# Kernel tuning notes

Measured on AMD Instinct MI355X. Metric: run time of the kernel, lower is better.

Reference implementation:

```python
import jax, jax.numpy as jnp
import numpy as np

BN_EPS = 1e-5

def _maxpool2x2(t):
    # t: [B, C, H, W] -> [B, C, H//2, W//2]
    B, C, H, W = t.shape
    return t.reshape(B, C, H // 2, 2, W // 2, 2).max(axis=(3, 5))

def setup_inputs() -> dict:
    key = jax.random.key(0)
    ks = jax.random.split(key, 7)
    B, C, D, H, W = 16, 256, 128, 64, 64
    return {
        "x": jax.random.normal(ks[0], (B, C, H, W), dtype=jnp.float32),
        "g_w": jax.random.normal(ks[1], (D, C), dtype=jnp.float32) * (1.0 / np.sqrt(C)),
        "g_b": jax.random.normal(ks[2], (D,), dtype=jnp.float32) * 0.01,
        "w_w": jax.random.normal(ks[3], (C, D), dtype=jnp.float32) * (1.0 / np.sqrt(D)),
        "w_b": jax.random.normal(ks[4], (C,), dtype=jnp.float32) * 0.01,
        "gamma": jax.random.normal(ks[5], (C,), dtype=jnp.float32),
        "beta": jax.random.normal(ks[6], (C,), dtype=jnp.float32),
    }

def reference(x, g_w, g_b, w_w, w_b, gamma, beta):
    B, C, H, W = x.shape
    D = g_w.shape[0]
    # g branch: 1x1 conv C->D then 2x2 maxpool, flatten -> [B, M, D]
    g_x = jnp.einsum('bchw,dc->bdhw', x, g_w) + g_b[None, :, None, None]
    g_x = _maxpool2x2(g_x).reshape(B, D, -1).transpose(0, 2, 1)      # [B, M, D]
    # theta: raw x flattened -> [B, N, C]; phi: maxpooled x -> [B, C, M]
    theta = x.reshape(B, C, -1).transpose(0, 2, 1)                    # [B, N, C]
    phi = _maxpool2x2(x).reshape(B, C, -1)                            # [B, C, M]
    f = jnp.einsum('bnc,bcm->bnm', theta, phi)                        # [B, N, M]
    attn = jax.nn.softmax(f, axis=-1)
    y = jnp.einsum('bnm,bmd->bnd', attn, g_x)                         # [B, N, D]
    y = y.transpose(0, 2, 1).reshape(B, D, H, W)
    # W: 1x1 conv D->C then BatchNorm2d (training mode: batch stats)
    w_y = jnp.einsum('bdhw,cd->bchw', y, w_w) + w_b[None, :, None, None]
    mean = w_y.mean(axis=(0, 2, 3))
    var = w_y.var(axis=(0, 2, 3))  # biased, matching torch BN normalization
    w_y = (w_y - mean[None, :, None, None]) * jax.lax.rsqrt(var + BN_EPS)[None, :, None, None]
    w_y = w_y * gamma[None, :, None, None] + beta[None, :, None, None]
    return w_y + x
```

## Files before the change

### kernel.cpp

```cpp
#include <hip/hip_runtime.h>
#include <hip/hip_bf16.h>

typedef _Float16 half8 __attribute__((ext_vector_type(8)));
typedef float f32x4 __attribute__((ext_vector_type(4)));
typedef unsigned uint4e __attribute__((ext_vector_type(4)));

#define B_ 16
#define C_ 256
#define D_ 128
#define H_ 64
#define W_ 64
#define N_ 4096
#define M_ 1024
#define NCH 32

static constexpr size_t WS_PHI   = 0;
static constexpr size_t WS_GPOOL = WS_PHI   + (size_t)B_*M_*C_*2;
static constexpr size_t WS_Y     = WS_GPOOL + (size_t)B_*D_*M_*2;
static constexpr size_t WS_BNSUM = WS_Y     + (size_t)B_*N_*D_*2;
static constexpr size_t WS_BNSSQ = WS_BNSUM + (size_t)C_*4;
static constexpr size_t WS_PSUM  = WS_BNSSQ + (size_t)C_*4;
static constexpr size_t WS_PSSQ  = WS_PSUM  + (size_t)256*256*4;
static constexpr size_t WS_GW16  = WS_PSSQ  + (size_t)256*256*4;
static constexpr size_t WS_WW16  = WS_GW16  + (size_t)D_*C_*2;

typedef __attribute__((address_space(3))) void lds_vt;
typedef const __attribute__((address_space(1))) void gbl_vt;

__device__ __forceinline__ void gl2lds16(const void* g, void* s) {
  __builtin_amdgcn_global_load_lds((gbl_vt*)g, (lds_vt*)s, 16, 0, 0);
}

__device__ __forceinline__ unsigned pkrtz(float a, float b) {
  auto v = __builtin_amdgcn_cvt_pkrtz(a, b);
  return __builtin_bit_cast(unsigned, v);
}

__global__ __launch_bounds__(256) void conv16_kernel(
    const float* __restrict__ gw, const float* __restrict__ ww,
    _Float16* __restrict__ gw16, _Float16* __restrict__ ww16) {
  const int i = blockIdx.x*256 + threadIdx.x;
  gw16[i] = (_Float16)gw[i];
  ww16[i] = (_Float16)ww[i];
}

__global__ __launch_bounds__(256) void fused_pre_kernel(
    const float* __restrict__ x, const _Float16* __restrict__ gw16,
    const float* __restrict__ g_b, _Float16* __restrict__ phi,
    _Float16* __restrict__ gpool) {
  const int i = blockIdx.x;
  const int b = blockIdx.y;
  const int t = threadIdx.x;
  const int w = t >> 6, l = t & 63, gq = l >> 4, c16 = l & 15;
  const float* xb = x + (size_t)b*C_*N_;

  f32x4 acc[8][2];
#pragma unroll
  for (int ds = 0; ds < 8; ++ds) {
    acc[ds][0] = (f32x4){0.f,0.f,0.f,0.f};
    acc[ds][1] = (f32x4){0.f,0.f,0.f,0.f};
  }

  const int n0 = i*128 + w*16 + c16;
  const int mrow = i*32 + w*8 + (c16 >> 1);

  for (int kk = 0; kk < 8; ++kk) {
    const int c0 = kk*32 + gq*8;
    half8 bf0, bf1;
#pragma unroll
    for (int j = 0; j < 8; ++j) {
      bf0[j] = (_Float16)xb[(size_t)(c0 + j)*N_ + n0];
      bf1[j] = (_Float16)xb[(size_t)(c0 + j)*N_ + n0 + 64];
    }
    half8 pk_;
#pragma unroll
    for (int j = 0; j < 8; ++j) {
      float v = fmaxf((float)bf0[j], (float)bf1[j]);
      v = fmaxf(v, __shfl_xor(v, 1, 64));
      pk_[j] = (_Float16)v;
    }
    if (!(l & 1))
      *(half8*)(phi + ((size_t)b*M_ + mrow)*C_ + c0) = pk_;
#pragma unroll
    for (int ds = 0; ds < 8; ++ds) {
      half8 af = *(const half8*)(gw16 + (size_t)(ds*16 + c16)*C_ + c0);
      acc[ds][0] = __builtin_amdgcn_mfma_f32_16x16x32_f16(af, bf0, acc[ds][0], 0, 0, 0);
      acc[ds][1] = __builtin_amdgcn_mfma_f32_16x16x32_f16(af, bf1, acc[ds][1], 0, 0, 0);
    }
  }

#pragma unroll
  for (int ds = 0; ds < 8; ++ds) {
#pragma unroll
    for (int r = 0; r < 4; ++r) {
      const int d = ds*16 + gq*4 + r;
      float v = fmaxf(acc[ds][0][r], acc[ds][1][r]);
      v = fmaxf(v, __shfl_xor(v, 1, 64));
      if (!(l & 1))
        gpool[((size_t)b*D_ + d)*M_ + mrow] = (_Float16)(v + g_b[d]);
    }
  }
}

__device__ __forceinline__ half8 build_pa(const float p0[4], const float p1[4], int gq) {
  unsigned d0 = pkrtz(p0[0], p0[1]);
  unsigned d1 = pkrtz(p0[2], p0[3]);
  unsigned e0 = pkrtz(p1[0], p1[1]);
  unsigned e1 = pkrtz(p1[2], p1[3]);
  unsigned D0 = __shfl_xor(d0, 16, 64), D1 = __shfl_xor(d1, 16, 64);
  unsigned E0 = __shfl_xor(e0, 16, 64), E1 = __shfl_xor(e1, 16, 64);
  const bool lo = gq < 2;
  unsigned s0 = lo ? e0 : d0, s1 = lo ? e1 : d1;
  unsigned s2 = lo ? E0 : D0, s3 = lo ? E1 : D1;
  unsigned R0 = __shfl_xor(s0, 32, 64), R1 = __shfl_xor(s1, 32, 64);
  unsigned R2 = __shfl_xor(s2, 32, 64), R3 = __shfl_xor(s3, 32, 64);
  uint4e u;
  u[0] = gq==0 ? d0 : gq==1 ? R2 : gq==2 ? R0 : E0;
  u[1] = gq==0 ? d1 : gq==1 ? R3 : gq==2 ? R1 : E1;
  u[2] = gq==0 ? D0 : gq==1 ? R0 : gq==2 ? R2 : e0;
  u[3] = gq==0 ? D1 : gq==1 ? R1 : gq==2 ? R3 : e1;
  return __builtin_bit_cast(half8, u);
}

__global__ __launch_bounds__(256, 2) void attn_kernel(
    const float* __restrict__ x, const _Float16* __restrict__ phi,
    const _Float16* __restrict__ gpool, _Float16* __restrict__ y) {
  const int nt = blockIdx.x;
  const int b  = blockIdx.y;
  const int t  = threadIdx.x;
  const int w = t >> 6, l = t & 63, gq = l >> 4, c16 = l & 15;
  const int nw = nt*128 + w*32;

  __shared__ alignas(16) _Float16 phi_s[2][32*256];
  __shared__ alignas(16) _Float16 gp_s[2][128*32];

  half8 qf[2][8];
#pragma unroll
  for (int rt = 0; rt < 2; ++rt) {
    const int nq = nw + rt*16 + c16;
#pragma unroll
    for (int kk = 0; kk < 8; ++kk) {
      const int cb = kk*32 + gq*8;
      half8 q;
#pragma unroll
      for (int j = 0; j < 8; ++j) q[j] = (_Float16)x[((size_t)b*C_ + cb + j)*N_ + nq];
      qf[rt][kk] = q;
    }
  }

  f32x4 yacc[2][8];
#pragma unroll
  for (int rt = 0; rt < 2; ++rt)
#pragma unroll
    for (int ds = 0; ds < 8; ++ds) yacc[rt][ds] = (f32x4){0.f,0.f,0.f,0.f};
  float m_run[2] = {-INFINITY, -INFINITY};
  float l_run[2] = {0.f, 0.f};

  const int lhi = l >> 5, l31 = l & 31;

  auto stage = [&](int buf, int ch2) {
    const int m0 = ch2 * 32;
#pragma unroll
    for (int jj = 0; jj < 4; ++jj) {
      const int j = w*4 + jj;
      const char* src = (const char*)phi + ((size_t)(b*M_ + m0 + l31))*512 + (2*j + lhi)*16;
      gl2lds16(src, (char*)&phi_s[buf][0] + j*1024);
    }
#pragma unroll
    for (int jj = 0; jj < 2; ++jj) {
      const int j = w*2 + jj;
      const char* src = (const char*)gpool + (((size_t)(b*D_ + (j&1)*64 + l))*M_ + m0)*2 + (j>>1)*16;
      gl2lds16(src, (char*)&gp_s[buf][0] + j*1024);
    }
  };

  stage(0, 0);

  const char* pAbase = (const char*)&phi_s[0][0] + gq*512 + c16*16;
  const char* pBbase = (const char*)&gp_s[0][0] + gq*2048 + c16*16;

  for (int ch = 0; ch < NCH; ++ch) {
    const int cur = ch & 1;
    if (ch + 1 < NCH) {
      stage(cur ^ 1, ch + 1);
      asm volatile("s_waitcnt vmcnt(6)" ::: "memory");
    } else {
      asm volatile("s_waitcnt vmcnt(0)" ::: "memory");
    }
    __builtin_amdgcn_s_barrier();
    asm volatile("" ::: "memory");

    f32x4 fS[2][2];
    fS[0][0] = (f32x4){0.f,0.f,0.f,0.f}; fS[0][1] = (f32x4){0.f,0.f,0.f,0.f};
    fS[1][0] = (f32x4){0.f,0.f,0.f,0.f}; fS[1][1] = (f32x4){0.f,0.f,0.f,0.f};
    const char* pA = pAbase + cur*16384;
    __builtin_amdgcn_s_setprio(1);
#pragma unroll
    for (int kk = 0; kk < 8; ++kk) {
      half8 a0 = *(const half8*)(pA + kk*2048);
      half8 a1 = *(const half8*)(pA + kk*2048 + 256);
      fS[0][0] = __builtin_amdgcn_mfma_f32_16x16x32_f16(a0, qf[0][kk], fS[0][0], 0, 0, 0);
      fS[1][0] = __builtin_amdgcn_mfma_f32_16x16x32_f16(a0, qf[1][kk], fS[1][0], 0, 0, 0);
      fS[0][1] = __builtin_amdgcn_mfma_f32_16x16x32_f16(a1, qf[0][kk], fS[0][1], 0, 0, 0);
      fS[1][1] = __builtin_amdgcn_mfma_f32_16x16x32_f16(a1, qf[1][kk], fS[1][1], 0, 0, 0);
    }
    __builtin_amdgcn_s_setprio(0);

    float cm[2];
#pragma unroll
    for (int rt = 0; rt < 2; ++rt) {
      float cmax = fS[rt][0][0];
#pragma unroll
      for (int mt = 0; mt < 2; ++mt)
#pragma unroll
        for (int r = 0; r < 4; ++r) cmax = fmaxf(cmax, fS[rt][mt][r]);
      cmax = fmaxf(cmax, __shfl_xor(cmax, 16, 64));
      cmax = fmaxf(cmax, __shfl_xor(cmax, 32, 64));
      cm[rt] = cmax;
    }
    const float grow = fmaxf(cm[0] - m_run[0], cm[1] - m_run[1]);
    if (__any(grow > 8.0f)) {
#pragma unroll
      for (int rt = 0; rt < 2; ++rt) {
        const float mn = fmaxf(m_run[rt], cm[rt]);
        const float sc = __expf(m_run[rt] - mn);
        m_run[rt] = mn;
        l_run[rt] *= sc;
        const int sci = __float_as_int(sc);
#pragma unroll
        for (int r = 0; r < 4; ++r) {
          const float scn = __int_as_float(__builtin_amdgcn_ds_bpermute(4*(gq*4 + r), sci));
#pragma unroll
          for (int ds = 0; ds < 8; ++ds) yacc[rt][ds][r] *= scn;
        }
      }
    }
    half8 pa[2];
#pragma unroll
    for (int rt = 0; rt < 2; ++rt) {
      float p0[4], p1[4];
      float rs = 0.f;
#pragma unroll
      for (int r = 0; r < 4; ++r) {
        p0[r] = __expf(fS[rt][0][r] - m_run[rt]);
        p1[r] = __expf(fS[rt][1][r] - m_run[rt]);
        rs += p0[r] + p1[r];
      }
      rs += __shfl_xor(rs, 16, 64);
      rs += __shfl_xor(rs, 32, 64);
      l_run[rt] += rs;
      pa[rt] = build_pa(p0, p1, gq);
    }

    const char* pB = pBbase + cur*8192;
    __builtin_amdgcn_s_setprio(1);
#pragma unroll
    for (int ds = 0; ds < 8; ++ds) {
      half8 bv = *(const half8*)(pB + ds*256);
      yacc[0][ds] = __builtin_amdgcn_mfma_f32_16x16x32_f16(pa[0], bv, yacc[0][ds], 0, 0, 0);
      yacc[1][ds] = __builtin_amdgcn_mfma_f32_16x16x32_f16(pa[1], bv, yacc[1][ds], 0, 0, 0);
    }
    __builtin_amdgcn_s_setprio(0);

    asm volatile("" ::: "memory");
    __builtin_amdgcn_s_barrier();
    asm volatile("" ::: "memory");
  }

#pragma unroll
  for (int rt = 0; rt < 2; ++rt) {
    const float inv = 1.0f / l_run[rt];
    const int invi = __float_as_int(inv);
#pragma unroll
    for (int r = 0; r < 4; ++r) {
      const float invn = __int_as_float(__builtin_amdgcn_ds_bpermute(4*(gq*4 + r), invi));
      const int n = nw + rt*16 + gq*4 + r;
      _Float16* yr = y + ((size_t)b*N_ + n)*D_ + c16;
#pragma unroll
      for (int ds = 0; ds < 8; ++ds) yr[ds*16] = (_Float16)(yacc[rt][ds][r] * invn);
    }
  }
}

__global__ __launch_bounds__(256) void stats_partial_kernel(
    const _Float16* __restrict__ y, const _Float16* __restrict__ ww16,
    const float* __restrict__ w_b, float* __restrict__ psum,
    float* __restrict__ pssq) {
  const int nt = blockIdx.x, b = blockIdx.y, t = threadIdx.x;
  const int w = t >> 6, l = t & 63, g = l >> 4, c16 = l & 15;

  float s_acc[4][4], q_acc[4][4], wb_r[4][4];
#pragma unroll
  for (int cs = 0; cs < 4; ++cs)
#pragma unroll
    for (int r = 0; r < 4; ++r) {
      s_acc[cs][r] = 0.f; q_acc[cs][r] = 0.f;
      wb_r[cs][r] = w_b[w*64 + cs*16 + g*4 + r];
    }

  for (int nb = 0; nb < 4; ++nb) {
    const int n0 = nt*256 + nb*64;
    f32x4 acc[4][4];
#pragma unroll
    for (int a = 0; a < 4; ++a)
#pragma unroll
      for (int n = 0; n < 4; ++n) acc[a][n] = (f32x4){0.f,0.f,0.f,0.f};

#pragma unroll
    for (int kk = 0; kk < 4; ++kk) {
      const int d0 = kk*32 + g*8;
      half8 af[4];
#pragma unroll
      for (int cs = 0; cs < 4; ++cs)
        af[cs] = *(const half8*)(ww16 + (size_t)(w*64 + cs*16 + c16)*D_ + d0);
#pragma unroll
      for (int ns = 0; ns < 4; ++ns) {
        const int nn = n0 + ns*16 + c16;
        half8 bf = *(const half8*)&y[((size_t)b*N_ + nn)*D_ + d0];
#pragma unroll
        for (int cs = 0; cs < 4; ++cs)
          acc[cs][ns] = __builtin_amdgcn_mfma_f32_16x16x32_f16(af[cs], bf, acc[cs][ns], 0, 0, 0);
      }
    }
#pragma unroll
    for (int cs = 0; cs < 4; ++cs)
#pragma unroll
      for (int r = 0; r < 4; ++r) {
        const float wb = wb_r[cs][r];
#pragma unroll
        for (int ns = 0; ns < 4; ++ns) {
          const float v = acc[cs][ns][r] + wb;
          s_acc[cs][r] += v; q_acc[cs][r] += v*v;
        }
      }
  }

  const int blk = b*16 + nt;
#pragma unroll
  for (int cs = 0; cs < 4; ++cs)
#pragma unroll
    for (int r = 0; r < 4; ++r) {
      float s = s_acc[cs][r], q = q_acc[cs][r];
      s += __shfl_xor(s, 1, 64); s += __shfl_xor(s, 2, 64);
      s += __shfl_xor(s, 4, 64); s += __shfl_xor(s, 8, 64);
      q += __shfl_xor(q, 1, 64); q += __shfl_xor(q, 2, 64);
      q += __shfl_xor(q, 4, 64); q += __shfl_xor(q, 8, 64);
      if (c16 == 0) {
        const int c = w*64 + cs*16 + g*4 + r;
        psum[blk*C_ + c] = s;
        pssq[blk*C_ + c] = q;
      }
    }
}

__global__ __launch_bounds__(256) void stats_reduce_kernel(
    const float* __restrict__ psum, const float* __restrict__ pssq,
    float* __restrict__ bnsum, float* __restrict__ bnssq) {
  const int t = threadIdx.x;
  const int ci = t & 31, bi = t >> 5;
  const int c = blockIdx.x*32 + ci;
  float s = 0.f, q = 0.f;
  for (int k = 0; k < 32; ++k) {
    const int row = bi + k*8;
    s += psum[row*C_ + c];
    q += pssq[row*C_ + c];
  }
  __shared__ float rs[8][32], rq[8][32];
  rs[bi][ci] = s; rq[bi][ci] = q;
  __syncthreads();
  if (bi == 0) {
    float S = 0.f, Q = 0.f;
#pragma unroll
    for (int k2 = 0; k2 < 8; ++k2) { S += rs[k2][ci]; Q += rq[k2][ci]; }
    bnsum[c] = S; bnssq[c] = Q;
  }
}

__global__ __launch_bounds__(256) void wconv_bn_kernel(
    const _Float16* __restrict__ y, const _Float16* __restrict__ ww16,
    const float* __restrict__ w_b, const float* __restrict__ bnsum,
    const float* __restrict__ bnssq, const float* __restrict__ gamma,
    const float* __restrict__ beta, const float* __restrict__ x,
    float* __restrict__ out) {
  const int nt = blockIdx.x, b = blockIdx.y, t = threadIdx.x;
  const int w = t >> 6, l = t & 63, g = l >> 4, c16 = l & 15;
  const int n0 = nt*64;

  f32x4 acc[4][4];
#pragma unroll
  for (int a = 0; a < 4; ++a)
#pragma unroll
    for (int n = 0; n < 4; ++n) acc[a][n] = (f32x4){0.f,0.f,0.f,0.f};

#pragma unroll
  for (int kk = 0; kk < 4; ++kk) {
    const int d0 = kk*32 + g*8;
    half8 af[4];
#pragma unroll
    for (int cs = 0; cs < 4; ++cs)
      af[cs] = *(const half8*)(ww16 + (size_t)(w*64 + cs*16 + c16)*D_ + d0);
#pragma unroll
    for (int ns = 0; ns < 4; ++ns) {
      const int nn = n0 + ns*16 + c16;
      half8 bf = *(const half8*)&y[((size_t)b*N_ + nn)*D_ + d0];
#pragma unroll
      for (int cs = 0; cs < 4; ++cs)
        acc[cs][ns] = __builtin_amdgcn_mfma_f32_16x16x32_f16(af[cs], bf, acc[cs][ns], 0, 0, 0);
    }
  }

  const float inv_cnt = 1.0f / (float)((size_t)B_ * N_);
#pragma unroll
  for (int cs = 0; cs < 4; ++cs) {
#pragma unroll
    for (int r = 0; r < 4; ++r) {
      const int c = w*64 + cs*16 + g*4 + r;
      const float wb  = w_b[c];
      const float mean = bnsum[c] * inv_cnt;
      const float var  = bnssq[c] * inv_cnt - mean*mean;
      const float istd = rsqrtf(var + 1e-5f);
      const float ga = gamma[c], be = beta[c];
#pragma unroll
      for (int ns = 0; ns < 4; ++ns) {
        const int n = n0 + ns*16 + c16;
        const size_t idx = ((size_t)b*C_ + c)*N_ + n;
        const float v = acc[cs][ns][r] + wb;
        out[idx] = (v - mean)*istd*ga + be + x[idx];
      }
    }
  }
}

extern "C" void kernel_launch(void* const* d_in, const int* in_sizes, int n_in,
                              void* d_out, int out_size, void* d_ws, size_t ws_size,
                              hipStream_t stream) {
  const float* x     = (const float*)d_in[0];
  const float* g_w   = (const float*)d_in[1];
  const float* g_b   = (const float*)d_in[2];
  const float* w_w   = (const float*)d_in[3];
  const float* w_b   = (const float*)d_in[4];
  const float* gamma = (const float*)d_in[5];
  const float* beta  = (const float*)d_in[6];
  float* out = (float*)d_out;

  char* ws = (char*)d_ws;
  _Float16* phi   = (_Float16*)(ws + WS_PHI);
  _Float16* gpool = (_Float16*)(ws + WS_GPOOL);
  _Float16* yb    = (_Float16*)(ws + WS_Y);
  float*    bnsum = (float*)(ws + WS_BNSUM);
  float*    bnssq = (float*)(ws + WS_BNSSQ);
  float*    psum  = (float*)(ws + WS_PSUM);
  float*    pssq  = (float*)(ws + WS_PSSQ);
  _Float16* gw16  = (_Float16*)(ws + WS_GW16);
  _Float16* ww16  = (_Float16*)(ws + WS_WW16);

  conv16_kernel<<<128, 256, 0, stream>>>(g_w, w_w, gw16, ww16);
  fused_pre_kernel<<<dim3(32, 16), 256, 0, stream>>>(x, gw16, g_b, phi, gpool);
  attn_kernel<<<dim3(32, 16), 256, 0, stream>>>(x, phi, gpool, yb);
  stats_partial_kernel<<<dim3(16, 16), 256, 0, stream>>>(yb, ww16, w_b, psum, pssq);
  stats_reduce_kernel<<<8, 256, 0, stream>>>(psum, pssq, bnsum, bnssq);
  wconv_bn_kernel<<<dim3(64, 16), 256, 0, stream>>>(yb, ww16, w_b, bnsum, bnssq, gamma, beta, x, out);
}
```

Before: 228.8 us.

## Double warps per block and shrink per-warp tiles across pre, attention and stats kernels

Result: slower. 283.2 us (+23.8%).

```diff
diff --git a/kernel.cpp b/kernel.cpp
--- a/kernel.cpp
+++ b/kernel.cpp
@@ -20,8 +20,8 @@
 static constexpr size_t WS_BNSUM = WS_Y     + (size_t)B_*N_*D_*2;
 static constexpr size_t WS_BNSSQ = WS_BNSUM + (size_t)C_*4;
 static constexpr size_t WS_PSUM  = WS_BNSSQ + (size_t)C_*4;
-static constexpr size_t WS_PSSQ  = WS_PSUM  + (size_t)256*256*4;
-static constexpr size_t WS_GW16  = WS_PSSQ  + (size_t)256*256*4;
+static constexpr size_t WS_PSSQ  = WS_PSUM  + (size_t)1024*256*4;
+static constexpr size_t WS_GW16  = WS_PSSQ  + (size_t)1024*256*4;
 static constexpr size_t WS_WW16  = WS_GW16  + (size_t)D_*C_*2;
 
 typedef __attribute__((address_space(3))) void lds_vt;
@@ -44,25 +44,26 @@
   ww16[i] = (_Float16)ww[i];
 }
 
-__global__ __launch_bounds__(256) void fused_pre_kernel(
+__global__ __launch_bounds__(512, 4) void fused_pre_kernel(
     const float* __restrict__ x, const _Float16* __restrict__ gw16,
     const float* __restrict__ g_b, _Float16* __restrict__ phi,
     _Float16* __restrict__ gpool) {
   const int i = blockIdx.x;
   const int b = blockIdx.y;
   const int t = threadIdx.x;
-  const int w = t >> 6, l = t & 63, gq = l >> 4, c16 = l & 15;
+  const int w = t >> 6, l = t & 63, gq = (l >> 4) & 3, c16 = l & 15;
+  const int wn = w & 3, wd = w >> 2;
   const float* xb = x + (size_t)b*C_*N_;
 
-  f32x4 acc[8][2];
-#pragma unroll
-  for (int ds = 0; ds < 8; ++ds) {
+  f32x4 acc[4][2];
+#pragma unroll
+  for (int ds = 0; ds < 4; ++ds) {
     acc[ds][0] = (f32x4){0.f,0.f,0.f,0.f};
     acc[ds][1] = (f32x4){0.f,0.f,0.f,0.f};
   }
 
-  const int n0 = i*128 + w*16 + c16;
-  const int mrow = i*32 + w*8 + (c16 >> 1);
+  const int n0 = i*128 + wn*16 + c16;
+  const int mrow = i*32 + wn*8 + (c16 >> 1);
 
   for (int kk = 0; kk < 8; ++kk) {
     const int c0 = kk*32 + gq*8;
@@ -72,28 +73,30 @@
       bf0[j] = (_Float16)xb[(size_t)(c0 + j)*N_ + n0];
       bf1[j] = (_Float16)xb[(size_t)(c0 + j)*N_ + n0 + 64];
     }
-    half8 pk_;
-#pragma unroll
-    for (int j = 0; j < 8; ++j) {
-      float v = fmaxf((float)bf0[j], (float)bf1[j]);
-      v = fmaxf(v, __shfl_xor(v, 1, 64));
-      pk_[j] = (_Float16)v;
-    }
-    if (!(l & 1))
-      *(half8*)(phi + ((size_t)b*M_ + mrow)*C_ + c0) = pk_;
-#pragma unroll
-    for (int ds = 0; ds < 8; ++ds) {
-      half8 af = *(const half8*)(gw16 + (size_t)(ds*16 + c16)*C_ + c0);
+    if (wd == 0) {
+      half8 pk_;
+#pragma unroll
+      for (int j = 0; j < 8; ++j) {
+        float v = fmaxf((float)bf0[j], (float)bf1[j]);
+        v = fmaxf(v, __shfl_xor(v, 1, 64));
+        pk_[j] = (_Float16)v;
+      }
+      if (!(l & 1))
+        *(half8*)(phi + ((size_t)b*M_ + mrow)*C_ + c0) = pk_;
+    }
+#pragma unroll
+    for (int ds = 0; ds < 4; ++ds) {
+      half8 af = *(const half8*)(gw16 + (size_t)((wd*4 + ds)*16 + c16)*C_ + c0);
       acc[ds][0] = __builtin_amdgcn_mfma_f32_16x16x32_f16(af, bf0, acc[ds][0], 0, 0, 0);
       acc[ds][1] = __builtin_amdgcn_mfma_f32_16x16x32_f16(af, bf1, acc[ds][1], 0, 0, 0);
     }
   }
 
 #pragma unroll
-  for (int ds = 0; ds < 8; ++ds) {
+  for (int ds = 0; ds < 4; ++ds) {
 #pragma unroll
     for (int r = 0; r < 4; ++r) {
-      const int d = ds*16 + gq*4 + r;
+      const int d = (wd*4 + ds)*16 + gq*4 + r;
       float v = fmaxf(acc[ds][0][r], acc[ds][1][r]);
       v = fmaxf(v, __shfl_xor(v, 1, 64));
       if (!(l & 1))
@@ -122,144 +125,120 @@
   return __builtin_bit_cast(half8, u);
 }
 
-__global__ __launch_bounds__(256, 2) void attn_kernel(
+__global__ __launch_bounds__(512, 4) void attn_kernel(
     const float* __restrict__ x, const _Float16* __restrict__ phi,
     const _Float16* __restrict__ gpool, _Float16* __restrict__ y) {
   const int nt = blockIdx.x;
   const int b  = blockIdx.y;
   const int t  = threadIdx.x;
-  const int w = t >> 6, l = t & 63, gq = l >> 4, c16 = l & 15;
-  const int nw = nt*128 + w*32;
+  const int w = t >> 6, l = t & 63, gq = (l >> 4) & 3, c16 = l & 15;
 
   __shared__ alignas(16) _Float16 phi_s[2][32*256];
-  __shared__ alignas(16) _Float16 gp_s[2][128*32];
-
-  half8 qf[2][8];
-#pragma unroll
-  for (int rt = 0; rt < 2; ++rt) {
-    const int nq = nw + rt*16 + c16;
+
+  half8 qf[8];
+  {
+    const int nq = nt*128 + w*16 + c16;
 #pragma unroll
     for (int kk = 0; kk < 8; ++kk) {
       const int cb = kk*32 + gq*8;
       half8 q;
 #pragma unroll
       for (int j = 0; j < 8; ++j) q[j] = (_Float16)x[((size_t)b*C_ + cb + j)*N_ + nq];
-      qf[rt][kk] = q;
-    }
-  }
-
-  f32x4 yacc[2][8];
-#pragma unroll
-  for (int rt = 0; rt < 2; ++rt)
-#pragma unroll
-    for (int ds = 0; ds < 8; ++ds) yacc[rt][ds] = (f32x4){0.f,0.f,0.f,0.f};
-  float m_run[2] = {-INFINITY, -INFINITY};
-  float l_run[2] = {0.f, 0.f};
+      qf[kk] = q;
+    }
+  }
+
+  f32x4 yacc[8];
+#pragma unroll
+  for (int ds = 0; ds < 8; ++ds) yacc[ds] = (f32x4){0.f,0.f,0.f,0.f};
+  float m_run = -INFINITY, l_run = 0.f;
 
   const int lhi = l >> 5, l31 = l & 31;
+  const _Float16* vbase = gpool + ((size_t)b*D_ + c16)*M_ + gq*8;
 
   auto stage = [&](int buf, int ch2) {
     const int m0 = ch2 * 32;
 #pragma unroll
-    for (int jj = 0; jj < 4; ++jj) {
-      const int j = w*4 + jj;
+    for (int jj = 0; jj < 2; ++jj) {
+      const int j = w*2 + jj;
       const char* src = (const char*)phi + ((size_t)(b*M_ + m0 + l31))*512 + (2*j + lhi)*16;
       gl2lds16(src, (char*)&phi_s[buf][0] + j*1024);
     }
-#pragma unroll
-    for (int jj = 0; jj < 2; ++jj) {
-      const int j = w*2 + jj;
-      const char* src = (const char*)gpool + (((size_t)(b*D_ + (j&1)*64 + l))*M_ + m0)*2 + (j>>1)*16;
-      gl2lds16(src, (char*)&gp_s[buf][0] + j*1024);
-    }
   };
 
   stage(0, 0);
 
   const char* pAbase = (const char*)&phi_s[0][0] + gq*512 + c16*16;
-  const char* pBbase = (const char*)&gp_s[0][0] + gq*2048 + c16*16;
 
   for (int ch = 0; ch < NCH; ++ch) {
     const int cur = ch & 1;
+    const int m0 = ch*32;
+
+    half8 vb[8];
+#pragma unroll
+    for (int ds = 0; ds < 8; ++ds)
+      vb[ds] = *(const half8*)(vbase + (size_t)(ds*16)*M_ + m0);
+    __builtin_amdgcn_sched_barrier(0);
+
     if (ch + 1 < NCH) {
       stage(cur ^ 1, ch + 1);
-      asm volatile("s_waitcnt vmcnt(6)" ::: "memory");
+      asm volatile("s_waitcnt vmcnt(10)" ::: "memory");
     } else {
-      asm volatile("s_waitcnt vmcnt(0)" ::: "memory");
+      asm volatile("s_waitcnt vmcnt(8)" ::: "memory");
     }
     __builtin_amdgcn_s_barrier();
     asm volatile("" ::: "memory");
 
-    f32x4 fS[2][2];
-    fS[0][0] = (f32x4){0.f,0.f,0.f,0.f}; fS[0][1] = (f32x4){0.f,0.f,0.f,0.f};
-    fS[1][0] = (f32x4){0.f,0.f,0.f,0.f}; fS[1][1] = (f32x4){0.f,0.f,0.f,0.f};
+    f32x4 fS[2];
+    fS[0] = (f32x4){0.f,0.f,0.f,0.f}; fS[1] = (f32x4){0.f,0.f,0.f,0.f};
     const char* pA = pAbase + cur*16384;
     __builtin_amdgcn_s_setprio(1);
 #pragma unroll
     for (int kk = 0; kk < 8; ++kk) {
       half8 a0 = *(const half8*)(pA + kk*2048);
       half8 a1 = *(const half8*)(pA + kk*2048 + 256);
-      fS[0][0] = __builtin_amdgcn_mfma_f32_16x16x32_f16(a0, qf[0][kk], fS[0][0], 0, 0, 0);
-      fS[1][0] = __builtin_amdgcn_mfma_f32_16x16x32_f16(a0, qf[1][kk], fS[1][0], 0, 0, 0);
-      fS[0][1] = __builtin_amdgcn_mfma_f32_16x16x32_f16(a1, qf[0][kk], fS[0][1], 0, 0, 0);
-      fS[1][1] = __builtin_amdgcn_mfma_f32_16x16x32_f16(a1, qf[1][kk], fS[1][1], 0, 0, 0);
+      fS[0] = __builtin_amdgcn_mfma_f32_16x16x32_f16(a0, qf[kk], fS[0], 0, 0, 0);
+      fS[1] = __builtin_amdgcn_mfma_f32_16x16x32_f16(a1, qf[kk], fS[1], 0, 0, 0);
     }
     __builtin_amdgcn_s_setprio(0);
 
-    float cm[2];
-#pragma unroll
-    for (int rt = 0; rt < 2; ++rt) {
-      float cmax = fS[rt][0][0];
-#pragma unroll
-      for (int mt = 0; mt < 2; ++mt)
-#pragma unroll
-        for (int r = 0; r < 4; ++r) cmax = fmaxf(cmax, fS[rt][mt][r]);
-      cmax = fmaxf(cmax, __shfl_xor(cmax, 16, 64));
-      cmax = fmaxf(cmax, __shfl_xor(cmax, 32, 64));
-      cm[rt] = cmax;
-    }
-    const float grow = fmaxf(cm[0] - m_run[0], cm[1] - m_run[1]);
-    if (__any(grow > 8.0f)) {
-#pragma unroll
-      for (int rt = 0; rt < 2; ++rt) {
-        const float mn = fmaxf(m_run[rt], cm[rt]);
-        const float sc = __expf(m_run[rt] - mn);
-        m_run[rt] = mn;
-        l_run[rt] *= sc;
-        const int sci = __float_as_int(sc);
-#pragma unroll
-        for (int r = 0; r < 4; ++r) {
-          const float scn = __int_as_float(__builtin_amdgcn_ds_bpermute(4*(gq*4 + r), sci));
-#pragma unroll
-          for (int ds = 0; ds < 8; ++ds) yacc[rt][ds][r] *= scn;
-        }
+    float cmax = fS[0][0];
+#pragma unroll
+    for (int mt = 0; mt < 2; ++mt)
+#pragma unroll
+      for (int r = 0; r < 4; ++r) cmax = fmaxf(cmax, fS[mt][r]);
+    cmax = fmaxf(cmax, __shfl_xor(cmax, 16, 64));
+    cmax = fmaxf(cmax, __shfl_xor(cmax, 32, 64));
+    if (__any(cmax - m_run > 8.0f)) {
+      const float mn = fmaxf(m_run, cmax);
+      const float sc = __expf(m_run - mn);
+      m_run = mn;
+      l_run *= sc;
+      const int sci = __float_as_int(sc);
+#pragma unroll
+      for (int r = 0; r < 4; ++r) {
+        const float scn = __int_as_float(__builtin_amdgcn_ds_bpermute(4*(gq*4 + r), sci));
+#pragma unroll
+        for (int ds = 0; ds < 8; ++ds) yacc[ds][r] *= scn;
       }
     }
-    half8 pa[2];
-#pragma unroll
-    for (int rt = 0; rt < 2; ++rt) {
-      float p0[4], p1[4];
-      float rs = 0.f;
-#pragma unroll
-      for (int r = 0; r < 4; ++r) {
-        p0[r] = __expf(fS[rt][0][r] - m_run[rt]);
-        p1[r] = __expf(fS[rt][1][r] - m_run[rt]);
-        rs += p0[r] + p1[r];
-      }
-      rs += __shfl_xor(rs, 16, 64);
-      rs += __shfl_xor(rs, 32, 64);
-      l_run[rt] += rs;
-      pa[rt] = build_pa(p0, p1, gq);
-    }
-
-    const char* pB = pBbase + cur*8192;
+    float p0[4], p1[4];
+    float rs = 0.f;
+#pragma unroll
+    for (int r = 0; r < 4; ++r) {
+      p0[r] = __expf(fS[0][r] - m_run);
+      p1[r] = __expf(fS[1][r] - m_run);
+      rs += p0[r] + p1[r];
+    }
+    rs += __shfl_xor(rs, 16, 64);
+    rs += __shfl_xor(rs, 32, 64);
+    l_run += rs;
+    half8 pa = build_pa(p0, p1, gq);
+
     __builtin_amdgcn_s_setprio(1);
 #pragma unroll
-    for (int ds = 0; ds < 8; ++ds) {
-      half8 bv = *(const half8*)(pB + ds*256);
-      yacc[0][ds] = __builtin_amdgcn_mfma_f32_16x16x32_f16(pa[0], bv, yacc[0][ds], 0, 0, 0);
-      yacc[1][ds] = __builtin_amdgcn_mfma_f32_16x16x32_f16(pa[1], bv, yacc[1][ds], 0, 0, 0);
-    }
+    for (int ds = 0; ds < 8; ++ds)
+      yacc[ds] = __builtin_amdgcn_mfma_f32_16x16x32_f16(pa, vb[ds], yacc[ds], 0, 0, 0);
     __builtin_amdgcn_s_setprio(0);
 
     asm volatile("" ::: "memory");
@@ -267,17 +246,16 @@
     asm volatile("" ::: "memory");
   }
 
-#pragma unroll
-  for (int rt = 0; rt < 2; ++rt) {
-    const float inv = 1.0f / l_run[rt];
+  {
+    const float inv = 1.0f / l_run;
     const int invi = __float_as_int(inv);
 #pragma unroll
     for (int r = 0; r < 4; ++r) {
       const float invn = __int_as_float(__builtin_amdgcn_ds_bpermute(4*(gq*4 + r), invi));
-      const int n = nw + rt*16 + gq*4 + r;
+      const int n = nt*128 + w*16 + gq*4 + r;
       _Float16* yr = y + ((size_t)b*N_ + n)*D_ + c16;
 #pragma unroll
-      for (int ds = 0; ds < 8; ++ds) yr[ds*16] = (_Float16)(yacc[rt][ds][r] * invn);
+      for (int ds = 0; ds < 8; ++ds) yr[ds*16] = (_Float16)(yacc[ds][r] * invn);
     }
   }
 }
@@ -288,65 +266,49 @@
     float* __restrict__ pssq) {
   const int nt = blockIdx.x, b = blockIdx.y, t = threadIdx.x;
   const int w = t >> 6, l = t & 63, g = l >> 4, c16 = l & 15;
-
-  float s_acc[4][4], q_acc[4][4], wb_r[4][4];
+  const int n0 = nt*64;
+
+  f32x4 acc[4][4];
+#pragma unroll
+  for (int a = 0; a < 4; ++a)
+#pragma unroll
+    for (int n = 0; n < 4; ++n) acc[a][n] = (f32x4){0.f,0.f,0.f,0.f};
+
+#pragma unroll
+  for (int kk = 0; kk < 4; ++kk) {
+    const int d0 = kk*32 + g*8;
+    half8 af[4];
+#pragma unroll
+    for (int cs = 0; cs < 4; ++cs)
+      af[cs] = *(const half8*)(ww16 + (size_t)(w*64 + cs*16 + c16)*D_ + d0);
+#pragma unroll
+    for (int ns = 0; ns < 4; ++ns) {
+      const int nn = n0 + ns*16 + c16;
+      half8 bf = *(const half8*)&y[((size_t)b*N_ + nn)*D_ + d0];
+#pragma unroll
+      for (int cs = 0; cs < 4; ++cs)
+        acc[cs][ns] = __builtin_amdgcn_mfma_f32_16x16x32_f16(af[cs], bf, acc[cs][ns], 0, 0, 0);
+    }
+  }
+
+  const int blk = b*64 + nt;
 #pragma unroll
   for (int cs = 0; cs < 4; ++cs)
 #pragma unroll
     for (int r = 0; r < 4; ++r) {
-      s_acc[cs][r] = 0.f; q_acc[cs][r] = 0.f;
-      wb_r[cs][r] = w_b[w*64 + cs*16 + g*4 + r];
-    }
-
-  for (int nb = 0; nb < 4; ++nb) {
-    const int n0 = nt*256 + nb*64;
-    f32x4 acc[4][4];
-#pragma unroll
-    for (int a = 0; a < 4; ++a)
-#pragma unroll
-      for (int n = 0; n < 4; ++n) acc[a][n] = (f32x4){0.f,0.f,0.f,0.f};
-
-#pragma unroll
-    for (int kk = 0; kk < 4; ++kk) {
-      const int d0 = kk*32 + g*8;
-      half8 af[4];
-#pragma unroll
-      for (int cs = 0; cs < 4; ++cs)
-        af[cs] = *(const half8*)(ww16 + (size_t)(w*64 + cs*16 + c16)*D_ + d0);
+      const int c = w*64 + cs*16 + g*4 + r;
+      const float wb = w_b[c];
+      float s = 0.f, q = 0.f;
 #pragma unroll
       for (int ns = 0; ns < 4; ++ns) {
-        const int nn = n0 + ns*16 + c16;
-        half8 bf = *(const half8*)&y[((size_t)b*N_ + nn)*D_ + d0];
-#pragma unroll
-        for (int cs = 0; cs < 4; ++cs)
-          acc[cs][ns] = __builtin_amdgcn_mfma_f32_16x16x32_f16(af[cs], bf, acc[cs][ns], 0, 0, 0);
+        const float v = acc[cs][ns][r] + wb;
+        s += v; q += v*v;
       }
-    }
-#pragma unroll
-    for (int cs = 0; cs < 4; ++cs)
-#pragma unroll
-      for (int r = 0; r < 4; ++r) {
-        const float wb = wb_r[cs][r];
-#pragma unroll
-        for (int ns = 0; ns < 4; ++ns) {
-          const float v = acc[cs][ns][r] + wb;
-          s_acc[cs][r] += v; q_acc[cs][r] += v*v;
-        }
-      }
-  }
-
-  const int blk = b*16 + nt;
-#pragma unroll
-  for (int cs = 0; cs < 4; ++cs)
-#pragma unroll
-    for (int r = 0; r < 4; ++r) {
-      float s = s_acc[cs][r], q = q_acc[cs][r];
       s += __shfl_xor(s, 1, 64); s += __shfl_xor(s, 2, 64);
       s += __shfl_xor(s, 4, 64); s += __shfl_xor(s, 8, 64);
       q += __shfl_xor(q, 1, 64); q += __shfl_xor(q, 2, 64);
       q += __shfl_xor(q, 4, 64); q += __shfl_xor(q, 8, 64);
       if (c16 == 0) {
-        const int c = w*64 + cs*16 + g*4 + r;
         psum[blk*C_ + c] = s;
         pssq[blk*C_ + c] = q;
       }
@@ -360,7 +322,7 @@
   const int ci = t & 31, bi = t >> 5;
   const int c = blockIdx.x*32 + ci;
   float s = 0.f, q = 0.f;
-  for (int k = 0; k < 32; ++k) {
+  for (int k = 0; k < 128; ++k) {
     const int row = bi + k*8;
     s += psum[row*C_ + c];
     q += pssq[row*C_ + c];
@@ -455,9 +417,9 @@
   _Float16* ww16  = (_Float16*)(ws + WS_WW16);
 
   conv16_kernel<<<128, 256, 0, stream>>>(g_w, w_w, gw16, ww16);
-  fused_pre_kernel<<<dim3(32, 16), 256, 0, stream>>>(x, gw16, g_b, phi, gpool);
-  attn_kernel<<<dim3(32, 16), 256, 0, stream>>>(x, phi, gpool, yb);
-  stats_partial_kernel<<<dim3(16, 16), 256, 0, stream>>>(yb, ww16, w_b, psum, pssq);
+  fused_pre_kernel<<<dim3(32, 16), 512, 0, stream>>>(x, gw16, g_b, phi, gpool);
+  attn_kernel<<<dim3(32, 16), 512, 0, stream>>>(x, phi, gpool, yb);
+  stats_partial_kernel<<<dim3(64, 16), 256, 0, stream>>>(yb, ww16, w_b, psum, pssq);
   stats_reduce_kernel<<<8, 256, 0, stream>>>(psum, pssq, bnsum, bnssq);
   wconv_bn_kernel<<<dim3(64, 16), 256, 0, stream>>>(yb, ww16, w_b, bnsum, bnssq, gamma, beta, x, out);
 }
```
